# Kernel optimization log

Hardware: AMD Instinct MI355X
Metric: run time of the kernel (lower is better)

## Reference

```python
import jax, jax.numpy as jnp
import numpy as np

B, N, F, L = 4, 8192, 64, 2


def setup_inputs() -> dict:
    key = jax.random.key(0)
    k1, k2, k3 = jax.random.split(key, 3)
    x = jax.random.normal(k1, (B, N, F), dtype=jnp.float32)
    net_params = jax.random.normal(k2, (L * F * F,), dtype=jnp.float32)
    A = jax.random.normal(k3, (N, N), dtype=jnp.float32)
    return {"x": x, "t": 0, "net_params": net_params, "A": A}


def reference(x, t, net_params, A):
    # weights: [L, F, F]
    weights = net_params.reshape(L, F, F)
    # x: [B, N, F] (original does x.view(-1, A.size(1), features))
    z = x.reshape(-1, A.shape[1], F)
    for i in range(L):
        # GCN_operation: Z_out = A @ Z @ W_i  (the nested vmm loops emulate exactly this)
        h = jnp.einsum('mn,bnf->bmf', A, z)          # [B, N, F]
        z = jnp.einsum('bmf,fg->bmg', h, weights[i])  # [B, N, F]
        z = jax.nn.relu(z)
    return z
```

## Files before the change

kernel.cpp:

```cpp
#include <hip/hip_runtime.h>
#include <stdint.h>


#define MK 8192

typedef float f32x4 __attribute__((ext_vector_type(4)));
typedef uint32_t u32x4 __attribute__((ext_vector_type(4)));
typedef uint32_t u32x2 __attribute__((ext_vector_type(2)));
typedef __bf16 bf16x8 __attribute__((ext_vector_type(8)));

__device__ inline uint16_t f2bf(float f) {
  uint32_t u = __builtin_bit_cast(uint32_t, f);
  u += 0x7fffu + ((u >> 16) & 1u);
  return (uint16_t)(u >> 16);
}
__device__ inline float bf2f(uint32_t lo16) {
  return __builtin_bit_cast(float, lo16 << 16);
}

#define GLD(src, dstbase)                                                                    \
  __builtin_amdgcn_global_load_lds((const __attribute__((address_space(1))) uint32_t*)(src), \
                                   (__attribute__((address_space(3))) uint32_t*)(dstbase),   \
                                   16, 0, 0)

__global__ __launch_bounds__(256) void zw0(const float* __restrict__ x,
                                           const float* __restrict__ net,
                                           uint16_t* __restrict__ Zt) {
  __shared__ float Wl[64 * 64];
  __shared__ float rows[64][65];
  const int b = blockIdx.y, n0 = blockIdx.x * 64, tid = threadIdx.x;
  for (int i = tid * 4; i < 4096; i += 1024) {
    f32x4 v = *(const f32x4*)(net + i);
    Wl[i] = v[0]; Wl[i + 1] = v[1]; Wl[i + 2] = v[2]; Wl[i + 3] = v[3];
  }
  const float* src = x + ((uint64_t)b * MK + n0) * 64;
  for (int i = tid * 4; i < 4096; i += 1024) {
    f32x4 v = *(const f32x4*)(src + i);
    int r = i >> 6, f = i & 63;
    rows[r][f] = v[0]; rows[r][f + 1] = v[1]; rows[r][f + 2] = v[2]; rows[r][f + 3] = v[3];
  }
  __syncthreads();
  const int nl = tid & 63, g0 = (tid >> 6) * 16;
  float s[16];
#pragma unroll
  for (int j = 0; j < 16; ++j) s[j] = 0.f;
  for (int f = 0; f < 64; ++f) {
    float rv = rows[nl][f];
#pragma unroll
    for (int j = 0; j < 16; ++j) s[j] = fmaf(rv, Wl[f * 64 + g0 + j], s[j]);
  }
  uint16_t* dst = Zt + (uint64_t)(b * 64 + g0) * MK + n0 + nl;
#pragma unroll
  for (int j = 0; j < 16; ++j) dst[(uint64_t)j * MK] = f2bf(s[j]);
}

__global__ __launch_bounds__(512, 2) void gemm1(const float* __restrict__ Af,
                                                const uint16_t* __restrict__ Bt,
                                                uint16_t* __restrict__ Ab,
                                                uint16_t* __restrict__ P) {
  __shared__ __align__(16) uint16_t As[2][16384];
  __shared__ __align__(16) uint16_t Bs[2][16384];
  const int bid = (int)blockIdx.x;
  const int s = bid & 7, bm = bid >> 3;
  const int row0 = bm * 256, k0 = s * 1024;
  const int tid = threadIdx.x, wid = tid >> 6, lane = tid & 63;
  const int wr = wid >> 2, wc = wid & 3;

  const int lsub = lane >> 3;
  const int ksrc = ((lane & 7) ^ lsub) << 3;
  const uint16_t* gB0 = Bt + (uint64_t)(4 * wid * 8 + lsub) * MK + k0 + ksrc;
  const int lBo = 4 * wid * 512;

  const int arow = (8 * wid) * 4 + (lane >> 4);
  const int acol = (lane & 15) * 4;
  const float* gA0 = Af + (uint64_t)(row0 + arow) * MK + k0 + acol;
  const int koct = (lane & 15) >> 1, krem = (lane & 1) * 4;

  f32x4 acc[8][4] = {};
  f32x4 rv[8];

  auto loadA = [&](int kofs) {
#pragma unroll
    for (int j = 0; j < 8; ++j)
      rv[j] = __builtin_nontemporal_load((const f32x4*)(gA0 + (uint64_t)j * 4 * MK + kofs));
  };
  auto stageA = [&](int buf, int kofs) {
#pragma unroll
    for (int j = 0; j < 8; ++j) {
      const int r = arow + j * 4;
      u32x2 w;
      w[0] = (uint32_t)f2bf(rv[j][0]) | ((uint32_t)f2bf(rv[j][1]) << 16);
      w[1] = (uint32_t)f2bf(rv[j][2]) | ((uint32_t)f2bf(rv[j][3]) << 16);
      *(u32x2*)&As[buf][r * 64 + ((koct ^ (r & 7)) << 3) + krem] = w;
      *(u32x2*)(Ab + (uint64_t)(row0 + r) * MK + k0 + kofs + acol) = w;
    }
  };

  loadA(0);
#pragma unroll
  for (int j = 0; j < 4; ++j) GLD(gB0 + (uint64_t)j * 8 * MK, &Bs[0][lBo + j * 512]);
  stageA(0, 0);
  __syncthreads();

  int buf = 0;
  for (int t = 0; t < 16; ++t) {
    const int nxt = (t + 1) * 64;
    if (t < 15) {
      loadA(nxt);
#pragma unroll
      for (int j = 0; j < 4; ++j) GLD(gB0 + (uint64_t)j * 8 * MK + nxt, &Bs[buf ^ 1][lBo + j * 512]);
    }
#pragma unroll
    for (int kk = 0; kk < 2; ++kk) {
      const int kb = kk * 4 + (lane >> 4);
      bf16x8 a[8], b[4];
#pragma unroll
      for (int mi = 0; mi < 8; ++mi) {
        const int r = wr * 128 + mi * 16 + (lane & 15);
        a[mi] = *(const bf16x8*)&As[buf][r * 64 + ((kb ^ (r & 7)) << 3)];
      }
#pragma unroll
      for (int n = 0; n < 4; ++n) {
        const int r = wc * 64 + n * 16 + (lane & 15);
        b[n] = *(const bf16x8*)&Bs[buf][r * 64 + ((kb ^ (r & 7)) << 3)];
      }
#pragma unroll
      for (int mi = 0; mi < 8; ++mi)
#pragma unroll
        for (int n = 0; n < 4; ++n)
          acc[mi][n] = __builtin_amdgcn_mfma_f32_16x16x32_bf16(a[mi], b[n], acc[mi][n], 0, 0, 0);
    }
    if (t < 15) stageA(buf ^ 1, nxt);
    __syncthreads();
    buf ^= 1;
  }

  uint16_t* Pp = P + (uint64_t)s * 2097152;
  const int lr = (lane >> 4) * 4, lc = lane & 15;
#pragma unroll
  for (int mi = 0; mi < 8; ++mi)
#pragma unroll
    for (int n = 0; n < 4; ++n) {
      const int gr = row0 + wr * 128 + mi * 16 + lr;
      const int gc = wc * 64 + n * 16 + lc;
#pragma unroll
      for (int j = 0; j < 4; ++j)
        Pp[(uint64_t)(gr + j) * 256 + gc] = f2bf(acc[mi][n][j]);
    }
}

__global__ __launch_bounds__(512, 2) void gemm2(const uint16_t* __restrict__ Ab,
                                                const uint16_t* __restrict__ Bt,
                                                uint16_t* __restrict__ P) {
  __shared__ __align__(16) uint16_t As[2][4096];
  __shared__ __align__(16) uint16_t Bs[2][8192];
  const int bid = (int)blockIdx.x;
  const int s = bid & 7, bm = bid >> 3;
  const int row0 = bm * 128, k0 = s * 1024;
  const int tid = threadIdx.x, wid = tid >> 6, lane = tid & 63;
  const int wr = wid >> 2, wc = wid & 3;

  const int crow = lane >> 2, coct = (lane & 3) * 8;
  const uint16_t* gA = Ab + (uint64_t)(row0 + wid * 16 + crow) * MK + k0 + coct;
  const uint16_t* gB0 = Bt + (uint64_t)(wid * 16 + crow) * MK + k0 + coct;
  const uint16_t* gB1 = Bt + (uint64_t)(128 + wid * 16 + crow) * MK + k0 + coct;
  const int lA = wid * 512, lB0 = wid * 512, lB1 = 4096 + wid * 512;

  f32x4 acc[4][4] = {};

  GLD(gA, &As[0][lA]);
  GLD(gB0, &Bs[0][lB0]);
  GLD(gB1, &Bs[0][lB1]);
  __syncthreads();

  int buf = 0;
  for (int t = 0; t < 32; ++t) {
    if (t < 31) {
      const int nxt = (t + 1) * 32;
      GLD(gA + nxt, &As[buf ^ 1][lA]);
      GLD(gB0 + nxt, &Bs[buf ^ 1][lB0]);
      GLD(gB1 + nxt, &Bs[buf ^ 1][lB1]);
    }
    bf16x8 a[4], b[4];
#pragma unroll
    for (int m = 0; m < 4; ++m)
      a[m] = *(const bf16x8*)&As[buf][(wr * 64 + m * 16 + (lane & 15)) * 32 + (lane >> 4) * 8];
#pragma unroll
    for (int n = 0; n < 4; ++n)
      b[n] = *(const bf16x8*)&Bs[buf][(wc * 64 + n * 16 + (lane & 15)) * 32 + (lane >> 4) * 8];
#pragma unroll
    for (int m = 0; m < 4; ++m)
#pragma unroll
      for (int n = 0; n < 4; ++n)
        acc[m][n] = __builtin_amdgcn_mfma_f32_16x16x32_bf16(a[m], b[n], acc[m][n], 0, 0, 0);
    __syncthreads();
    buf ^= 1;
  }

  uint16_t* Pp = P + (uint64_t)s * 2097152;
  const int lr = (lane >> 4) * 4, lc = lane & 15;
#pragma unroll
  for (int m = 0; m < 4; ++m)
#pragma unroll
    for (int n = 0; n < 4; ++n) {
      const int gr = row0 + wr * 64 + m * 16 + lr;
      const int gc = wc * 64 + n * 16 + lc;
#pragma unroll
      for (int j = 0; j < 4; ++j)
        Pp[(uint64_t)(gr + j) * 256 + gc] = f2bf(acc[m][n][j]);
    }
}

__global__ __launch_bounds__(256) void zw1P(const uint16_t* __restrict__ P,
                                            const float* __restrict__ net,
                                            uint16_t* __restrict__ Zt) {
  __shared__ float Wl[64 * 64];
  __shared__ float rows[64][65];
  const int b = blockIdx.y, n0 = blockIdx.x * 64, tid = threadIdx.x;
  const float* Wsrc = net + 4096;
  for (int i = tid * 4; i < 4096; i += 1024) {
    f32x4 v = *(const f32x4*)(Wsrc + i);
    Wl[i] = v[0]; Wl[i + 1] = v[1]; Wl[i + 2] = v[2]; Wl[i + 3] = v[3];
  }
#pragma unroll
  for (int g = 0; g < 2; ++g) {
    const int idx = (tid + g * 256) * 8;
    const int r = idx >> 6, f0 = idx & 63;
    const uint16_t* base = P + (uint64_t)(n0 + r) * 256 + b * 64 + f0;
    float acc8[8] = {};
#pragma unroll
    for (int sp = 0; sp < 8; ++sp) {
      u32x4 v = *(const u32x4*)(base + (uint64_t)sp * 2097152);
#pragma unroll
      for (int j = 0; j < 4; ++j) {
        acc8[2 * j]     += bf2f(v[j] & 0xffffu);
        acc8[2 * j + 1] += bf2f(v[j] >> 16);
      }
    }
#pragma unroll
    for (int j = 0; j < 8; ++j) rows[r][f0 + j] = fmaxf(acc8[j], 0.0f);
  }
  __syncthreads();
  const int nl = tid & 63, g0 = (tid >> 6) * 16;
  float s[16];
#pragma unroll
  for (int j = 0; j < 16; ++j) s[j] = 0.f;
  for (int f = 0; f < 64; ++f) {
    float rv = rows[nl][f];
#pragma unroll
    for (int j = 0; j < 16; ++j) s[j] = fmaf(rv, Wl[f * 64 + g0 + j], s[j]);
  }
  uint16_t* dst = Zt + (uint64_t)(b * 64 + g0) * MK + n0 + nl;
#pragma unroll
  for (int j = 0; j < 16; ++j) dst[(uint64_t)j * MK] = f2bf(s[j]);
}

__global__ __launch_bounds__(256) void combineF(const uint16_t* __restrict__ P,
                                                float* __restrict__ out) {
  const uint64_t e = ((uint64_t)blockIdx.x * 256 + threadIdx.x) * 8;
  float acc8[8] = {};
#pragma unroll
  for (int sp = 0; sp < 8; ++sp) {
    u32x4 v = *(const u32x4*)&P[(uint64_t)sp * 2097152 + e];
#pragma unroll
    for (int j = 0; j < 4; ++j) {
      acc8[2 * j]     += bf2f(v[j] & 0xffffu);
      acc8[2 * j + 1] += bf2f(v[j] >> 16);
    }
  }
  const int m = (int)(e >> 8);
  const int c = (int)(e & 255);
  float* dst = &out[(((uint64_t)(c >> 6)) * MK + m) * 64 + (c & 63)];
  f32x4 w0, w1;
#pragma unroll
  for (int j = 0; j < 4; ++j) { w0[j] = fmaxf(acc8[j], 0.0f); w1[j] = fmaxf(acc8[4 + j], 0.0f); }
  *(f32x4*)dst = w0;
  *(f32x4*)(dst + 4) = w1;
}

extern "C" void kernel_launch(void* const* d_in, const int* in_sizes, int n_in,
                              void* d_out, int out_size, void* d_ws, size_t ws_size,
                              hipStream_t stream) {
  const float* x   = (const float*)d_in[0];
  const float* net = (const float*)d_in[2];
  const float* A   = (const float*)d_in[3];
  float* out = (float*)d_out;

  uint16_t* Ab = (uint16_t*)d_ws;
  uint16_t* Zt = (uint16_t*)((char*)d_ws + 134217728ull);
  uint16_t* P  = (uint16_t*)((char*)d_ws + 142606336ull);

  zw0<<<dim3(128, 4), dim3(256), 0, stream>>>(x, net, Zt);
  gemm1<<<dim3(256), dim3(512), 0, stream>>>(A, Zt, Ab, P);
  zw1P<<<dim3(128, 4), dim3(256), 0, stream>>>(P, net, Zt);
  gemm2<<<dim3(512), dim3(512), 0, stream>>>(Ab, Zt, P);
  combineF<<<dim3(1024), dim3(256), 0, stream>>>(P, out);
}
```

Baseline: 178.5 us.

## Split A fp32-to-bf16 conversion into its own kernel and share one GEMM kernel

A new kernel converts A from fp32 to bf16 up front. The first GEMM previously did this conversion inline while writing Ab as a side effect. Both GEMM passes now run one kernel that loads A and B tiles straight into LDS with async global-to-LDS loads. The second pass changes from a 128-row, 32-wide-k tiling to the 256-row, 64-wide-k tiling. The aim is a cleaner, fully async pipeline for both GEMMs, at the cost of an extra full pass that reads A in fp32 and writes it as bf16.

```diff
diff --git a/kernel.cpp b/kernel.cpp
--- a/kernel.cpp
+++ b/kernel.cpp
@@ -22,6 +22,22 @@
   __builtin_amdgcn_global_load_lds((const __attribute__((address_space(1))) uint32_t*)(src), \
                                    (__attribute__((address_space(3))) uint32_t*)(dstbase),   \
                                    16, 0, 0)
+
+__global__ __launch_bounds__(256) void cvtA(const float* __restrict__ A, uint16_t* __restrict__ Ab) {
+  const uint64_t total = (uint64_t)MK * MK;
+  uint64_t i = ((uint64_t)blockIdx.x * 256 + threadIdx.x) * 8;
+  const uint64_t stride = (uint64_t)gridDim.x * 256 * 8;
+  for (; i < total; i += stride) {
+    f32x4 v0 = __builtin_nontemporal_load((const f32x4*)(A + i));
+    f32x4 v1 = __builtin_nontemporal_load((const f32x4*)(A + i + 4));
+    u32x4 w;
+    w[0] = (uint32_t)f2bf(v0[0]) | ((uint32_t)f2bf(v0[1]) << 16);
+    w[1] = (uint32_t)f2bf(v0[2]) | ((uint32_t)f2bf(v0[3]) << 16);
+    w[2] = (uint32_t)f2bf(v1[0]) | ((uint32_t)f2bf(v1[1]) << 16);
+    w[3] = (uint32_t)f2bf(v1[2]) | ((uint32_t)f2bf(v1[3]) << 16);
+    *(u32x4*)(Ab + i) = w;
+  }
+}
 
 __global__ __launch_bounds__(256) void zw0(const float* __restrict__ x,
                                            const float* __restrict__ net,
@@ -54,10 +70,9 @@
   for (int j = 0; j < 16; ++j) dst[(uint64_t)j * MK] = f2bf(s[j]);
 }
 
-__global__ __launch_bounds__(512, 2) void gemm1(const float* __restrict__ Af,
-                                                const uint16_t* __restrict__ Bt,
-                                                uint16_t* __restrict__ Ab,
-                                                uint16_t* __restrict__ P) {
+__global__ __launch_bounds__(512, 2) void gemm(const uint16_t* __restrict__ Ab,
+                                               const uint16_t* __restrict__ Bt,
+                                               uint16_t* __restrict__ P) {
   __shared__ __align__(16) uint16_t As[2][16384];
   __shared__ __align__(16) uint16_t Bs[2][16384];
   const int bid = (int)blockIdx.x;
@@ -68,47 +83,28 @@
 
   const int lsub = lane >> 3;
   const int ksrc = ((lane & 7) ^ lsub) << 3;
+  const uint16_t* gA0 = Ab + (uint64_t)(row0 + 4 * wid * 8 + lsub) * MK + k0 + ksrc;
   const uint16_t* gB0 = Bt + (uint64_t)(4 * wid * 8 + lsub) * MK + k0 + ksrc;
-  const int lBo = 4 * wid * 512;
-
-  const int arow = (8 * wid) * 4 + (lane >> 4);
-  const int acol = (lane & 15) * 4;
-  const float* gA0 = Af + (uint64_t)(row0 + arow) * MK + k0 + acol;
-  const int koct = (lane & 15) >> 1, krem = (lane & 1) * 4;
+  const int lo = 4 * wid * 512;
 
   f32x4 acc[8][4] = {};
-  f32x4 rv[8];
-
-  auto loadA = [&](int kofs) {
-#pragma unroll
-    for (int j = 0; j < 8; ++j)
-      rv[j] = __builtin_nontemporal_load((const f32x4*)(gA0 + (uint64_t)j * 4 * MK + kofs));
-  };
-  auto stageA = [&](int buf, int kofs) {
-#pragma unroll
-    for (int j = 0; j < 8; ++j) {
-      const int r = arow + j * 4;
-      u32x2 w;
-      w[0] = (uint32_t)f2bf(rv[j][0]) | ((uint32_t)f2bf(rv[j][1]) << 16);
-      w[1] = (uint32_t)f2bf(rv[j][2]) | ((uint32_t)f2bf(rv[j][3]) << 16);
-      *(u32x2*)&As[buf][r * 64 + ((koct ^ (r & 7)) << 3) + krem] = w;
-      *(u32x2*)(Ab + (uint64_t)(row0 + r) * MK + k0 + kofs + acol) = w;
-    }
-  };
-
-  loadA(0);
-#pragma unroll
-  for (int j = 0; j < 4; ++j) GLD(gB0 + (uint64_t)j * 8 * MK, &Bs[0][lBo + j * 512]);
-  stageA(0, 0);
+
+#pragma unroll
+  for (int j = 0; j < 4; ++j) {
+    GLD(gA0 + (uint64_t)j * 8 * MK, &As[0][lo + j * 512]);
+    GLD(gB0 + (uint64_t)j * 8 * MK, &Bs[0][lo + j * 512]);
+  }
   __syncthreads();
 
   int buf = 0;
   for (int t = 0; t < 16; ++t) {
-    const int nxt = (t + 1) * 64;
     if (t < 15) {
-      loadA(nxt);
-#pragma unroll
-      for (int j = 0; j < 4; ++j) GLD(gB0 + (uint64_t)j * 8 * MK + nxt, &Bs[buf ^ 1][lBo + j * 512]);
+      const int nxt = (t + 1) * 64;
+#pragma unroll
+      for (int j = 0; j < 4; ++j) {
+        GLD(gA0 + (uint64_t)j * 8 * MK + nxt, &As[buf ^ 1][lo + j * 512]);
+        GLD(gB0 + (uint64_t)j * 8 * MK + nxt, &Bs[buf ^ 1][lo + j * 512]);
+      }
     }
 #pragma unroll
     for (int kk = 0; kk < 2; ++kk) {
@@ -130,7 +126,6 @@
         for (int n = 0; n < 4; ++n)
           acc[mi][n] = __builtin_amdgcn_mfma_f32_16x16x32_bf16(a[mi], b[n], acc[mi][n], 0, 0, 0);
     }
-    if (t < 15) stageA(buf ^ 1, nxt);
     __syncthreads();
     buf ^= 1;
   }
@@ -146,68 +141,6 @@
 #pragma unroll
       for (int j = 0; j < 4; ++j)
         Pp[(uint64_t)(gr + j) * 256 + gc] = f2bf(acc[mi][n][j]);
-    }
-}
-
-__global__ __launch_bounds__(512, 2) void gemm2(const uint16_t* __restrict__ Ab,
-                                                const uint16_t* __restrict__ Bt,
-                                                uint16_t* __restrict__ P) {
-  __shared__ __align__(16) uint16_t As[2][4096];
-  __shared__ __align__(16) uint16_t Bs[2][8192];
-  const int bid = (int)blockIdx.x;
-  const int s = bid & 7, bm = bid >> 3;
-  const int row0 = bm * 128, k0 = s * 1024;
-  const int tid = threadIdx.x, wid = tid >> 6, lane = tid & 63;
-  const int wr = wid >> 2, wc = wid & 3;
-
-  const int crow = lane >> 2, coct = (lane & 3) * 8;
-  const uint16_t* gA = Ab + (uint64_t)(row0 + wid * 16 + crow) * MK + k0 + coct;
-  const uint16_t* gB0 = Bt + (uint64_t)(wid * 16 + crow) * MK + k0 + coct;
-  const uint16_t* gB1 = Bt + (uint64_t)(128 + wid * 16 + crow) * MK + k0 + coct;
-  const int lA = wid * 512, lB0 = wid * 512, lB1 = 4096 + wid * 512;
-
-  f32x4 acc[4][4] = {};
-
-  GLD(gA, &As[0][lA]);
-  GLD(gB0, &Bs[0][lB0]);
-  GLD(gB1, &Bs[0][lB1]);
-  __syncthreads();
-
-  int buf = 0;
-  for (int t = 0; t < 32; ++t) {
-    if (t < 31) {
-      const int nxt = (t + 1) * 32;
-      GLD(gA + nxt, &As[buf ^ 1][lA]);
-      GLD(gB0 + nxt, &Bs[buf ^ 1][lB0]);
-      GLD(gB1 + nxt, &Bs[buf ^ 1][lB1]);
-    }
-    bf16x8 a[4], b[4];
-#pragma unroll
-    for (int m = 0; m < 4; ++m)
-      a[m] = *(const bf16x8*)&As[buf][(wr * 64 + m * 16 + (lane & 15)) * 32 + (lane >> 4) * 8];
-#pragma unroll
-    for (int n = 0; n < 4; ++n)
-      b[n] = *(const bf16x8*)&Bs[buf][(wc * 64 + n * 16 + (lane & 15)) * 32 + (lane >> 4) * 8];
-#pragma unroll
-    for (int m = 0; m < 4; ++m)
-#pragma unroll
-      for (int n = 0; n < 4; ++n)
-        acc[m][n] = __builtin_amdgcn_mfma_f32_16x16x32_bf16(a[m], b[n], acc[m][n], 0, 0, 0);
-    __syncthreads();
-    buf ^= 1;
-  }
-
-  uint16_t* Pp = P + (uint64_t)s * 2097152;
-  const int lr = (lane >> 4) * 4, lc = lane & 15;
-#pragma unroll
-  for (int m = 0; m < 4; ++m)
-#pragma unroll
-    for (int n = 0; n < 4; ++n) {
-      const int gr = row0 + wr * 64 + m * 16 + lr;
-      const int gc = wc * 64 + n * 16 + lc;
-#pragma unroll
-      for (int j = 0; j < 4; ++j)
-        Pp[(uint64_t)(gr + j) * 256 + gc] = f2bf(acc[m][n][j]);
     }
 }
 
@@ -290,9 +223,10 @@
   uint16_t* Zt = (uint16_t*)((char*)d_ws + 134217728ull);
   uint16_t* P  = (uint16_t*)((char*)d_ws + 142606336ull);
 
+  cvtA<<<dim3(2048), dim3(256), 0, stream>>>(A, Ab);
   zw0<<<dim3(128, 4), dim3(256), 0, stream>>>(x, net, Zt);
-  gemm1<<<dim3(256), dim3(512), 0, stream>>>(A, Zt, Ab, P);
+  gemm<<<dim3(256), dim3(512), 0, stream>>>(Ab, Zt, P);
   zw1P<<<dim3(128, 4), dim3(256), 0, stream>>>(P, net, Zt);
-  gemm2<<<dim3(512), dim3(512), 0, stream>>>(Ab, Zt, P);
+  gemm<<<dim3(256), dim3(512), 0, stream>>>(Ab, Zt, P);
   combineF<<<dim3(1024), dim3(256), 0, stream>>>(P, out);
 }
```

Result: no change. 178.7 us (+0.1%).
